# Optimization experiments

Hardware: AMD Instinct MI355X
Metric: run time of the kernel (lower is better)

Reference implementation:

```python
import jax, jax.numpy as jnp
import numpy as np

GROUP_SIZE = 16777216   # 2**24, output length
PROJ_RATIO = 0.25
INNER = 4194304         # int(GROUP_SIZE * PROJ_RATIO) = 2**22
PADDED = 16777216       # 2**ceil(log2(GROUP_SIZE)) = 2**24
D = 2048                # int(sqrt(INNER))
RANK = 16
ALPHA = 1.0
SCALING = ALPHA / RANK


def setup_inputs() -> dict:
    key = jax.random.key(0)
    kA, kB = jax.random.split(key)
    # LoRA factors (B is zero-init in torch; use small random values so the
    # pipeline produces non-trivial numbers — the math is identical).
    A = jax.random.normal(kA, (RANK, D), dtype=jnp.float32) * 0.02
    Bw = jax.random.normal(kB, (D, RANK), dtype=jnp.float32) * 0.02
    # Fastfood buffers, deterministic as in FastfoodProjection(seed=42)
    rng = np.random.RandomState(42)
    G = jnp.asarray(rng.randn(PADDED), dtype=jnp.float32)
    sign = jnp.asarray(rng.choice([-1, 1], size=PADDED), dtype=jnp.float32)
    perm = jnp.asarray(rng.permutation(PADDED), dtype=jnp.int32)
    return {"A": A, "Bw": Bw, "G": G, "sign": sign, "perm": perm}


def fwht(x):
    """Fast Walsh-Hadamard transform over the last (only) axis, normalized
    by 1/sqrt(n). Same butterfly order as the torch loop: step doubles from 1,
    within each block of 2*step: (a, b) -> (a+b, a-b)."""
    n = x.shape[-1]  # static python int, power of two
    step = 1
    while step < n:
        y = x.reshape(-1, 2, step)               # blocks of 2*step
        x = jnp.concatenate([y[:, :1] + y[:, 1:], y[:, :1] - y[:, 1:]],
                            axis=1).reshape(-1)
        step *= 2
    return x * np.float32(1.0 / np.sqrt(n))


def reference(A, Bw, G, sign, perm):
    # LoRA delta: (D, RANK) @ (RANK, D) * alpha/rank -> (D, D)
    delta = (Bw @ A) * jnp.float32(SCALING)
    flat = delta.reshape(-1)                     # (INNER,)
    flat = jnp.pad(flat, (0, PADDED - INNER))    # zero-pad to 2**24
    # Fastfood: H * G * Pi * H * B
    out = fwht(flat * sign)
    out = out[perm] * G
    out = fwht(out)
    # out_features == GROUP_SIZE == PADDED, so the slice/pad in
    # SuperLoRAGroup.forward is a no-op here; keep it for faithfulness.
    return out[:GROUP_SIZE]
```

## Files before the change

kernel.cpp:

```cpp
#include <hip/hip_runtime.h>


#define THREADS 1024

typedef float vf4 __attribute__((ext_vector_type(4)));
typedef int vi4 __attribute__((ext_vector_type(4)));

constexpr float kScaling = 0.0625f;
constexpr float kNorm = 5.9604644775390625e-8f;

__device__ __forceinline__ void fwht16(float r[16]) {
#pragma unroll
  for (int s = 1; s < 16; s <<= 1) {
#pragma unroll
    for (int i = 0; i < 16; i++) {
      if (!(i & s)) {
        float a = r[i];
        float b = r[i | s];
        r[i] = a + b;
        r[i | s] = a - b;
      }
    }
  }
}

template <bool NT>
__device__ __forceinline__ void fwht_lo_rounds(float* lds, int t, vf4* dst4) {
  vf4* lds4 = (vf4*)lds;
  {
    float r[16];
#pragma unroll
    for (int q = 0; q < 4; q++) {
      vf4 v = lds4[t * 4 + q];
#pragma unroll
      for (int c = 0; c < 4; c++) r[4 * q + c] = v[c];
    }
    fwht16(r);
#pragma unroll
    for (int q = 0; q < 4; q++) {
      vf4 v;
#pragma unroll
      for (int c = 0; c < 4; c++) v[c] = r[4 * q + c];
      lds4[t * 4 + q] = v;
    }
  }
  __syncthreads();
  {
    const int c = (t & 15) | ((t >> 4) << 8);
    float r[16];
#pragma unroll
    for (int k = 0; k < 16; k++) r[k] = lds[c + (k << 4)];
    fwht16(r);
#pragma unroll
    for (int k = 0; k < 16; k++) lds[c + (k << 4)] = r[k];
  }
  __syncthreads();
  {
    const int c = (t & 255) | ((t >> 8) << 12);
    float r[16];
#pragma unroll
    for (int k = 0; k < 16; k++) r[k] = lds[c + (k << 8)];
    fwht16(r);
#pragma unroll
    for (int k = 0; k < 16; k++) lds[c + (k << 8)] = r[k];
  }
  __syncthreads();
  {
    vf4 v0 = lds4[t + 0 * 1024];
    vf4 v1 = lds4[t + 1 * 1024];
    vf4 v2 = lds4[t + 2 * 1024];
    vf4 v3 = lds4[t + 3 * 1024];
    vf4 e0 = v0 + v1, e1 = v0 - v1;
    vf4 e2 = v2 + v3, e3 = v2 - v3;
    vf4 o0 = e0 + e2, o1 = e1 + e3, o2 = e0 - e2, o3 = e1 - e3;
    if (NT) {
      __builtin_nontemporal_store(o0, &dst4[t + 0 * 1024]);
      __builtin_nontemporal_store(o1, &dst4[t + 1 * 1024]);
      __builtin_nontemporal_store(o2, &dst4[t + 2 * 1024]);
      __builtin_nontemporal_store(o3, &dst4[t + 3 * 1024]);
    } else {
      dst4[t + 0 * 1024] = o0;
      dst4[t + 1 * 1024] = o1;
      dst4[t + 2 * 1024] = o2;
      dst4[t + 3 * 1024] = o3;
    }
  }
}

__global__ __launch_bounds__(THREADS) void k1_build_fwht_lo(
    const float* __restrict__ A, const float* __restrict__ Bw,
    const float* __restrict__ sgn, float* __restrict__ W) {
  __shared__ float lds[16384];
  const int t = threadIdx.x;
  const int blk = blockIdx.x;
  const unsigned base = (unsigned)blk << 14;

  float a0[16], a1[16];
#pragma unroll
  for (int k = 0; k < 16; k++) {
    a0[k] = A[k * 2048 + t];
    a1[k] = A[k * 2048 + t + 1024];
  }
  const int r0 = blk * 8;
#pragma unroll
  for (int rl = 0; rl < 8; rl++) {
    float s0 = 0.f, s1 = 0.f;
#pragma unroll
    for (int k = 0; k < 16; k++) {
      float b = Bw[(r0 + rl) * 16 + k];
      s0 += b * a0[k];
      s1 += b * a1[k];
    }
    const int l0 = rl * 2048 + t;
    const int l1 = l0 + 1024;
    lds[l0] = s0 * kScaling * sgn[base + l0];
    lds[l1] = s1 * kScaling * sgn[base + l1];
  }
  __syncthreads();
  fwht_lo_rounds<false>(lds, t, (vf4*)W + ((unsigned)blk << 12));
}

__global__ __launch_bounds__(THREADS) void k_fwht_mid(float* __restrict__ buf) {
  __shared__ float lds[16384];
  vf4* lds4 = (vf4*)lds;
  const int t = threadIdx.x;
  const int seg = blockIdx.x >> 8;
  const int c0 = (blockIdx.x & 255) * 16;
  vf4* B4 = (vf4*)buf + ((unsigned)seg << 20);
#pragma unroll
  for (int m = 0; m < 4; m++) {
    const int idx4 = t + THREADS * m;
    const int row = idx4 >> 4, c4 = idx4 & 15;
    lds4[idx4] = B4[row * 4096 + c0 + c4];
  }
  __syncthreads();
  const int c4 = t & 15;
  const int f = t >> 4;
#pragma unroll
  for (int r = 0; r < 4; r++) {
    const int m = 1 << (2 * r);
    int rows[4];
#pragma unroll
    for (int k2 = 0; k2 < 4; k2++)
      rows[k2] = (f & (m - 1)) + k2 * m + (f >> (2 * r)) * (m << 2);
    vf4 v0 = lds4[rows[0] * 16 + c4];
    vf4 v1 = lds4[rows[1] * 16 + c4];
    vf4 v2 = lds4[rows[2] * 16 + c4];
    vf4 v3 = lds4[rows[3] * 16 + c4];
    vf4 e0 = v0 + v1, e1 = v0 - v1;
    vf4 e2 = v2 + v3, e3 = v2 - v3;
    vf4 o0 = e0 + e2, o1 = e1 + e3, o2 = e0 - e2, o3 = e1 - e3;
    if (r < 3) {
      lds4[rows[0] * 16 + c4] = o0;
      lds4[rows[1] * 16 + c4] = o1;
      lds4[rows[2] * 16 + c4] = o2;
      lds4[rows[3] * 16 + c4] = o3;
      __syncthreads();
    } else {
      B4[rows[0] * 4096 + c0 + c4] = o0;
      B4[rows[1] * 4096 + c0 + c4] = o1;
      B4[rows[2] * 4096 + c0 + c4] = o2;
      B4[rows[3] * 4096 + c0 + c4] = o3;
    }
  }
}

__global__ __launch_bounds__(THREADS, 8) void k3_perm_fwht_lo(
    const float* __restrict__ W, const int* __restrict__ perm,
    const float* __restrict__ G, float* __restrict__ out) {
  __shared__ float lds[16384];
  vf4* lds4 = (vf4*)lds;
  const int t = threadIdx.x;
  const unsigned base4 = (unsigned)blockIdx.x << 12;
  const vi4* P4 = (const vi4*)perm + base4;
  const vf4* G4 = (const vf4*)G + base4;
  int src[16];
#pragma unroll
  for (int m = 0; m < 4; m++) {
    const int idx4 = t + THREADS * m;
    vi4 p = __builtin_nontemporal_load(&P4[idx4]);
    vf4 g = __builtin_nontemporal_load(&G4[idx4]);
#pragma unroll
    for (int c = 0; c < 4; c++) src[4 * m + c] = p[c] & 0x3FFFFF;
    lds4[idx4] = g * kNorm;
  }
  float wv[16];
#pragma unroll
  for (int pass = 0; pass < 4; pass++) {
#pragma unroll
    for (int s = 0; s < 16; s++) {
      if ((src[s] >> 20) == pass) wv[s] = W[src[s]];
    }
    if (pass < 3) {
      asm volatile("s_waitcnt vmcnt(8)" ::: "memory");
      __builtin_amdgcn_s_barrier();
    }
  }
#pragma unroll
  for (int m = 0; m < 4; m++) {
    vf4 v = lds4[t + THREADS * m];
#pragma unroll
    for (int c = 0; c < 4; c++) v[c] *= wv[4 * m + c];
    lds4[t + THREADS * m] = v;
  }
  __syncthreads();
  fwht_lo_rounds<true>(lds, t, (vf4*)out + base4);
}

__global__ __launch_bounds__(THREADS, 8) void k4_fwht_hi(float* __restrict__ out) {
  __shared__ float lds[16384];
  vf4* lds4 = (vf4*)lds;
  const int t = threadIdx.x;
  const unsigned blk = (blockIdx.x & 7) * 128u + (blockIdx.x >> 3);
  const unsigned c0 = blk * 4u;
  vf4* O4 = (vf4*)out;
#pragma unroll
  for (int m = 0; m < 4; m++) {
    const int idx4 = t + THREADS * m;
    const int row = idx4 >> 2, c4 = idx4 & 3;
    lds4[idx4 ^ ((idx4 >> 4) & 7)] = O4[(unsigned)row * 4096u + c0 + c4];
  }
  __syncthreads();
  const int c4 = t & 3;
  const int f = t >> 2;
#pragma unroll
  for (int r = 0; r < 5; r++) {
    const int m = 1 << (2 * r);
    int rows[4];
#pragma unroll
    for (int k = 0; k < 4; k++)
      rows[k] = (f & (m - 1)) + k * m + (f >> (2 * r)) * (m << 2);
    int sidx[4];
#pragma unroll
    for (int k = 0; k < 4; k++) {
      const int fidx = rows[k] * 4 + c4;
      sidx[k] = fidx ^ ((fidx >> 4) & 7);
    }
    vf4 v0 = lds4[sidx[0]];
    vf4 v1 = lds4[sidx[1]];
    vf4 v2 = lds4[sidx[2]];
    vf4 v3 = lds4[sidx[3]];
    vf4 e0 = v0 + v1, e1 = v0 - v1;
    vf4 e2 = v2 + v3, e3 = v2 - v3;
    vf4 o0 = e0 + e2, o1 = e1 + e3, o2 = e0 - e2, o3 = e1 - e3;
    if (r < 4) {
      lds4[sidx[0]] = o0;
      lds4[sidx[1]] = o1;
      lds4[sidx[2]] = o2;
      lds4[sidx[3]] = o3;
      __syncthreads();
    } else {
      __builtin_nontemporal_store(o0, &O4[(unsigned)rows[0] * 4096u + c0 + c4]);
      __builtin_nontemporal_store(o1, &O4[(unsigned)rows[1] * 4096u + c0 + c4]);
      __builtin_nontemporal_store(o2, &O4[(unsigned)rows[2] * 4096u + c0 + c4]);
      __builtin_nontemporal_store(o3, &O4[(unsigned)rows[3] * 4096u + c0 + c4]);
    }
  }
}

extern "C" void kernel_launch(void* const* d_in, const int* in_sizes, int n_in,
                              void* d_out, int out_size, void* d_ws,
                              size_t ws_size, hipStream_t stream) {
  (void)in_sizes;
  (void)n_in;
  (void)out_size;
  (void)ws_size;
  const float* A = (const float*)d_in[0];
  const float* Bw = (const float*)d_in[1];
  const float* G = (const float*)d_in[2];
  const float* sgn = (const float*)d_in[3];
  const int* perm = (const int*)d_in[4];
  float* out = (float*)d_out;
  float* W = (float*)d_ws;

  k1_build_fwht_lo<<<256, THREADS, 0, stream>>>(A, Bw, sgn, W);
  k_fwht_mid<<<256, THREADS, 0, stream>>>(W);
  k3_perm_fwht_lo<<<1024, THREADS, 0, stream>>>(W, perm, G, out);
  k4_fwht_hi<<<1024, THREADS, 0, stream>>>(out);
}
```

Measured before the change: 354.0 us.

## Restructure high-bit FWHT kernel into register radix-4 plus LDS stages, split gather passes

k4_fwht_hi now uses 512-thread blocks that each own 8 vf4 columns across all four 2^20 segments. The top radix-4 butterfly across segments is done in registers, and the remaining 8 bits are done in LDS one segment at a time. This replaces the 4096-row strided column tile and XOR swizzle, giving wider contiguous column reads (8 vf4 per row) and a smaller LDS footprint. Separately, the permutation gather in k3 is split into 8 passes of 2^19 elements with a tighter vmcnt wait, to improve L2 locality, at the cost of more barriers and less memory-level parallelism.

```diff
diff --git a/kernel.cpp b/kernel.cpp
--- a/kernel.cpp
+++ b/kernel.cpp
@@ -2,6 +2,7 @@
 
 
 #define THREADS 1024
+#define K4_THREADS 512
 
 typedef float vf4 __attribute__((ext_vector_type(4)));
 typedef int vi4 __attribute__((ext_vector_type(4)));
@@ -186,13 +187,13 @@
   }
   float wv[16];
 #pragma unroll
-  for (int pass = 0; pass < 4; pass++) {
+  for (int pass = 0; pass < 8; pass++) {
 #pragma unroll
     for (int s = 0; s < 16; s++) {
-      if ((src[s] >> 20) == pass) wv[s] = W[src[s]];
-    }
-    if (pass < 3) {
-      asm volatile("s_waitcnt vmcnt(8)" ::: "memory");
+      if ((src[s] >> 19) == pass) wv[s] = W[src[s]];
+    }
+    if (pass < 7) {
+      asm volatile("s_waitcnt vmcnt(4)" ::: "memory");
       __builtin_amdgcn_s_barrier();
     }
   }
@@ -207,53 +208,68 @@
   fwht_lo_rounds<true>(lds, t, (vf4*)out + base4);
 }
 
-__global__ __launch_bounds__(THREADS, 8) void k4_fwht_hi(float* __restrict__ out) {
-  __shared__ float lds[16384];
-  vf4* lds4 = (vf4*)lds;
-  const int t = threadIdx.x;
-  const unsigned blk = (blockIdx.x & 7) * 128u + (blockIdx.x >> 3);
-  const unsigned c0 = blk * 4u;
+__global__ __launch_bounds__(K4_THREADS, 4) void k4_fwht_hi(
+    float* __restrict__ out) {
+  __shared__ vf4 lds4[2048];
+  const int t = threadIdx.x;
+  const unsigned c04 = (unsigned)blockIdx.x * 8u;
   vf4* O4 = (vf4*)out;
-#pragma unroll
-  for (int m = 0; m < 4; m++) {
-    const int idx4 = t + THREADS * m;
-    const int row = idx4 >> 2, c4 = idx4 & 3;
-    lds4[idx4 ^ ((idx4 >> 4) & 7)] = O4[(unsigned)row * 4096u + c0 + c4];
-  }
-  __syncthreads();
-  const int c4 = t & 3;
-  const int f = t >> 2;
-#pragma unroll
-  for (int r = 0; r < 5; r++) {
-    const int m = 1 << (2 * r);
-    int rows[4];
-#pragma unroll
-    for (int k = 0; k < 4; k++)
-      rows[k] = (f & (m - 1)) + k * m + (f >> (2 * r)) * (m << 2);
-    int sidx[4];
-#pragma unroll
-    for (int k = 0; k < 4; k++) {
-      const int fidx = rows[k] * 4 + c4;
-      sidx[k] = fidx ^ ((fidx >> 4) & 7);
-    }
-    vf4 v0 = lds4[sidx[0]];
-    vf4 v1 = lds4[sidx[1]];
-    vf4 v2 = lds4[sidx[2]];
-    vf4 v3 = lds4[sidx[3]];
-    vf4 e0 = v0 + v1, e1 = v0 - v1;
-    vf4 e2 = v2 + v3, e3 = v2 - v3;
-    vf4 o0 = e0 + e2, o1 = e1 + e3, o2 = e0 - e2, o3 = e1 - e3;
-    if (r < 4) {
-      lds4[sidx[0]] = o0;
-      lds4[sidx[1]] = o1;
-      lds4[sidx[2]] = o2;
-      lds4[sidx[3]] = o3;
-      __syncthreads();
-    } else {
-      __builtin_nontemporal_store(o0, &O4[(unsigned)rows[0] * 4096u + c0 + c4]);
-      __builtin_nontemporal_store(o1, &O4[(unsigned)rows[1] * 4096u + c0 + c4]);
-      __builtin_nontemporal_store(o2, &O4[(unsigned)rows[2] * 4096u + c0 + c4]);
-      __builtin_nontemporal_store(o3, &O4[(unsigned)rows[3] * 4096u + c0 + c4]);
+
+  vf4 a[4][4];
+#pragma unroll
+  for (int s = 0; s < 4; s++) {
+#pragma unroll
+    for (int m = 0; m < 4; m++) {
+      const int idx4 = t + K4_THREADS * m;
+      const int row = idx4 >> 3, c4 = idx4 & 7;
+      a[s][m] =
+          O4[((unsigned)s << 20) + (unsigned)row * 4096u + c04 + (unsigned)c4];
+    }
+  }
+#pragma unroll
+  for (int m = 0; m < 4; m++) {
+    vf4 e0 = a[0][m] + a[1][m], e1 = a[0][m] - a[1][m];
+    vf4 e2 = a[2][m] + a[3][m], e3 = a[2][m] - a[3][m];
+    a[0][m] = e0 + e2;
+    a[1][m] = e1 + e3;
+    a[2][m] = e0 - e2;
+    a[3][m] = e1 - e3;
+  }
+  const int c4 = t & 7;
+  const int f = t >> 3;
+#pragma unroll
+  for (int s = 0; s < 4; s++) {
+    if (s) __syncthreads();
+#pragma unroll
+    for (int m = 0; m < 4; m++) lds4[t + K4_THREADS * m] = a[s][m];
+    __syncthreads();
+#pragma unroll
+    for (int r = 0; r < 4; r++) {
+      const int mm = 1 << (2 * r);
+      int rows[4];
+#pragma unroll
+      for (int k = 0; k < 4; k++)
+        rows[k] = (f & (mm - 1)) + k * mm + (f >> (2 * r)) * (mm << 2);
+      vf4 v0 = lds4[rows[0] * 8 + c4];
+      vf4 v1 = lds4[rows[1] * 8 + c4];
+      vf4 v2 = lds4[rows[2] * 8 + c4];
+      vf4 v3 = lds4[rows[3] * 8 + c4];
+      vf4 e0 = v0 + v1, e1 = v0 - v1;
+      vf4 e2 = v2 + v3, e3 = v2 - v3;
+      vf4 o0 = e0 + e2, o1 = e1 + e3, o2 = e0 - e2, o3 = e1 - e3;
+      if (r < 3) {
+        lds4[rows[0] * 8 + c4] = o0;
+        lds4[rows[1] * 8 + c4] = o1;
+        lds4[rows[2] * 8 + c4] = o2;
+        lds4[rows[3] * 8 + c4] = o3;
+        __syncthreads();
+      } else {
+        const unsigned sb = ((unsigned)s << 20) + c04 + (unsigned)c4;
+        __builtin_nontemporal_store(o0, &O4[sb + (unsigned)rows[0] * 4096u]);
+        __builtin_nontemporal_store(o1, &O4[sb + (unsigned)rows[1] * 4096u]);
+        __builtin_nontemporal_store(o2, &O4[sb + (unsigned)rows[2] * 4096u]);
+        __builtin_nontemporal_store(o3, &O4[sb + (unsigned)rows[3] * 4096u]);
+      }
     }
   }
 }
@@ -276,5 +292,5 @@
   k1_build_fwht_lo<<<256, THREADS, 0, stream>>>(A, Bw, sgn, W);
   k_fwht_mid<<<256, THREADS, 0, stream>>>(W);
   k3_perm_fwht_lo<<<1024, THREADS, 0, stream>>>(W, perm, G, out);
-  k4_fwht_hi<<<1024, THREADS, 0, stream>>>(out);
-}
+  k4_fwht_hi<<<512, K4_THREADS, 0, stream>>>(out);
+}
```

Result: no change. 351.6 us (-0.7%).
